# Kernel optimization log

Hardware: AMD Instinct MI355X
Metric: run time of the kernel (lower is better)

Reference implementation:

```python
import jax, jax.numpy as jnp
import numpy as np

EMBED_DIM = 1024
NUM_HEADS = 16
HEAD_DIM = EMBED_DIM // NUM_HEADS  # 64
SCALING = 0.125
T, B = 2048, 2


def setup_inputs() -> dict:
    key = jax.random.key(0)
    k_q, k_len, k_w1, k_b1, k_w2, k_b2 = jax.random.split(key, 6)
    query = jax.random.normal(k_q, (T, B, EMBED_DIM), dtype=jnp.float32)
    # realistic padding: each sequence has a valid length in [T//2, T)
    lengths = jax.random.randint(k_len, (B,), T // 2, T)
    key_padding_mask = jnp.arange(T)[None, :] >= lengths[:, None]  # [B, T] bool, True = pad
    s1 = 1.0 / np.sqrt(EMBED_DIM)
    W_in = jax.random.uniform(k_w1, (3 * EMBED_DIM, EMBED_DIM), jnp.float32, -s1, s1)
    b_in = jax.random.uniform(k_b1, (3 * EMBED_DIM,), jnp.float32, -s1, s1)
    W_out = jax.random.uniform(k_w2, (EMBED_DIM, EMBED_DIM), jnp.float32, -s1, s1)
    b_out = jax.random.uniform(k_b2, (EMBED_DIM,), jnp.float32, -s1, s1)
    return {"query": query, "key_padding_mask": key_padding_mask,
            "W_in": W_in, "b_in": b_in, "W_out": W_out, "b_out": b_out}


def reference(query, key_padding_mask, W_in, b_in, W_out, b_out):
    # query: [T, B, E]; key_padding_mask: [B, S] bool (True = padded key)
    t, b, e = query.shape
    h, hd = NUM_HEADS, HEAD_DIM
    proj = query @ W_in.T + b_in                      # [T, B, 3E]
    q, k, v = jnp.split(proj, 3, axis=-1)             # each [T, B, E]
    q = q * SCALING

    def to_bh(x):  # [T, B, E] -> [B*H, T, hd], matching torch view+transpose
        return x.reshape(t, b * h, hd).transpose(1, 0, 2)

    q, k, v = to_bh(q), to_bh(k), to_bh(v)
    attn_weights = jnp.einsum('bth,bsh->bts', q, k)   # [B*H, T, S]
    attn_weights = attn_weights.reshape(b, h, t, t)
    attn_weights = jnp.where(key_padding_mask[:, None, None, :], -jnp.inf, attn_weights)
    # softmax computed in float32 then cast back, as in the original
    attn_weights = jax.nn.softmax(attn_weights.astype(jnp.float32), axis=-1).astype(query.dtype)
    # dropout p=0 (eval/inference) -> identity
    attn = jnp.einsum('bhts,bhsd->bhtd', attn_weights, v.reshape(b, h, t, hd))  # [B,H,T,hd]
    attn = attn.reshape(b * h, t, hd).transpose(1, 0, 2).reshape(t, b, e)       # [T,B,E]
    return attn @ W_out.T + b_out
```

## Files before the change

### kernel.cpp

```cpp
#include <hip/hip_runtime.h>
#include <hip/hip_bf16.h>
#include <stdint.h>
#include <stddef.h>

typedef __hip_bfloat16 bf16;
typedef __attribute__((ext_vector_type(4))) float f32x4;
typedef __attribute__((ext_vector_type(8))) short s16x8;
typedef __attribute__((ext_vector_type(4))) short s16x4;

#define AS1 __attribute__((address_space(1)))
#define AS3 __attribute__((address_space(3)))

__device__ __forceinline__ void async_ld16(const void* g, void* l) {
  __builtin_amdgcn_global_load_lds((AS1 void*)g, (AS3 void*)l, 16, 0, 0);
}

#if __has_builtin(__builtin_amdgcn_exp2f)
#define EXP2F(x) __builtin_amdgcn_exp2f(x)
#else
#define EXP2F(x) exp2f(x)
#endif

__device__ __forceinline__ unsigned pk_bf16(float a, float b) {
  unsigned ua = __builtin_bit_cast(unsigned, a);
  unsigned ub = __builtin_bit_cast(unsigned, b);
  ua += 0x7FFFu + ((ua >> 16) & 1u);
  ub += 0x7FFFu + ((ub >> 16) & 1u);
  return (ua >> 16) | (ub & 0xFFFF0000u);
}

__device__ __forceinline__ unsigned pk_trunc(float a, float b) {
  return __builtin_amdgcn_perm(__builtin_bit_cast(unsigned, b),
                               __builtin_bit_cast(unsigned, a), 0x07060302u);
}

__global__ __launch_bounds__(256) void convert_all_kernel(const float* __restrict__ q_src,
                                                          const float* __restrict__ wi_src,
                                                          const float* __restrict__ wo_src,
                                                          bf16* __restrict__ q_dst,
                                                          bf16* __restrict__ wi_dst,
                                                          bf16* __restrict__ wo_dst,
                                                          const void* __restrict__ mask,
                                                          int* __restrict__ lengths) {
  int blk = blockIdx.x;
  if (blk >= 4096) {
    __shared__ int s_any;
    __shared__ int s_cnt[256];
    const int tid = threadIdx.x;
    const int b = blk - 4096;
    const unsigned char* m8 = (const unsigned char*)mask;
    if (tid == 0) s_any = 0;
    __syncthreads();
    int local = 0;
    for (int i = tid; i < 4096; i += 256) local |= m8[i];
    if (local) atomicOr(&s_any, 1);
    __syncthreads();
    int cnt = 0;
    if (s_any) {
      for (int t = tid; t < 2048; t += 256) cnt += (m8[b * 2048 + t] == 0) ? 1 : 0;
    } else {
      const int* m32 = (const int*)mask;
      for (int t = tid; t < 2048; t += 256) cnt += (m32[b * 2048 + t] == 0) ? 1 : 0;
    }
    s_cnt[tid] = cnt;
    __syncthreads();
    for (int s = 128; s > 0; s >>= 1) {
      if (tid < s) s_cnt[tid] += s_cnt[tid + s];
      __syncthreads();
    }
    if (tid == 0) lengths[b] = s_cnt[0];
    return;
  }
  const float* src;
  bf16* dst;
  int base;
  if (blk < 2048)      { src = q_src;  dst = q_dst;  base = blk * 2048; }
  else if (blk < 3584) { src = wi_src; dst = wi_dst; base = (blk - 2048) * 2048; }
  else                 { src = wo_src; dst = wo_dst; base = (blk - 3584) * 2048; }
  int i = base + threadIdx.x * 8;
  float4 a = *(const float4*)(src + i);
  float4 b = *(const float4*)(src + i + 4);
  unsigned u[4];
  u[0] = pk_bf16(a.x, a.y); u[1] = pk_bf16(a.z, a.w);
  u[2] = pk_bf16(b.x, b.y); u[3] = pk_bf16(b.z, b.w);
  *(uint4*)(dst + i) = *(const uint4*)u;
}

__global__ __launch_bounds__(256) void gemm_qkv(const bf16* __restrict__ X,
                                                const bf16* __restrict__ W,
                                                const float* __restrict__ bias,
                                                bf16* __restrict__ Qd,
                                                bf16* __restrict__ Kd,
                                                bf16* __restrict__ Vt) {
  __shared__ bf16 smem[128 * 64 * 2];
  bf16* As = smem;
  bf16* Bs = smem + 8192;
  const int K = 1024;
  const int id = blockIdx.x;
  const int xcd = id & 7;
  const int local = id >> 3;
  const int nloc = local % 3;
  const int by = local / 3;
  const int m0 = by * 128;
  const int n0 = (xcd * 3 + nloc) * 128;
  const int tid = threadIdx.x;
  const int wave = tid >> 6, lane = tid & 63;
  const int col = lane & 15, quad = lane >> 4;
  const int wm = wave & 1, wn = wave >> 1;

  f32x4 acc[4][4];
#pragma unroll
  for (int mi = 0; mi < 4; mi++)
#pragma unroll
    for (int ni = 0; ni < 4; ni++) acc[mi][ni] = (f32x4){0.f, 0.f, 0.f, 0.f};

  const bf16* gA[4];
  const bf16* gB[4];
  char* ldA[4];
  char* ldB[4];
#pragma unroll
  for (int i = 0; i < 4; i++) {
    const int c = tid + 256 * i;
    const int row = c >> 3;
    const int j = (c & 7) ^ (row & 7);
    gA[i] = X + (size_t)(m0 + row) * K + j * 8;
    gB[i] = W + (size_t)(n0 + row) * K + j * 8;
    ldA[i] = (char*)As + (size_t)(wave * 64 + 256 * i) * 16;
    ldB[i] = (char*)Bs + (size_t)(wave * 64 + 256 * i) * 16;
  }

  for (int k0 = 0; k0 < K; k0 += 64) {
#pragma unroll
    for (int i = 0; i < 4; i++) async_ld16(gA[i] + k0, ldA[i]);
#pragma unroll
    for (int i = 0; i < 4; i++) async_ld16(gB[i] + k0, ldB[i]);
    __syncthreads();
#pragma unroll
    for (int kh = 0; kh < 2; kh++) {
      s16x8 af[4], bfr[4];
#pragma unroll
      for (int mi = 0; mi < 4; mi++) {
        const int row = wm * 64 + mi * 16 + col;
        af[mi] = *(const s16x8*)((char*)As + row * 128 + (((kh << 2) | quad) ^ (row & 7)) * 16);
      }
#pragma unroll
      for (int ni = 0; ni < 4; ni++) {
        const int row = wn * 64 + ni * 16 + col;
        bfr[ni] = *(const s16x8*)((char*)Bs + row * 128 + (((kh << 2) | quad) ^ (row & 7)) * 16);
      }
#pragma unroll
      for (int mi = 0; mi < 4; mi++)
#pragma unroll
        for (int ni = 0; ni < 4; ni++)
          acc[mi][ni] = __builtin_amdgcn_mfma_f32_16x16x32_bf16(af[mi], bfr[ni], acc[mi][ni], 0, 0, 0);
    }
    __syncthreads();
  }

  const float QSCALE = 0.125f * 1.4426950408889634f;
  if (n0 < 2048) {
    bf16* dstb = (n0 < 1024) ? Qd : Kd;
    const float sc = (n0 < 1024) ? QSCALE : 1.0f;
#pragma unroll
    for (int mi = 0; mi < 4; mi++)
#pragma unroll
      for (int ni = 0; ni < 4; ni++)
#pragma unroll
        for (int r = 0; r < 4; r++) {
          int m = m0 + wm * 64 + mi * 16 + quad * 4 + r;
          int n = n0 + wn * 64 + ni * 16 + col;
          float v = (acc[mi][ni][r] + bias[n]) * sc;
          int e = n & 1023, hh = e >> 6, d = e & 63;
          int t = m >> 1, b = m & 1;
          int bh = b * 16 + hh;
          dstb[((size_t)bh * 2048 + t) * 64 + d] = __float2bfloat16(v);
        }
  } else {
    const int hh0 = (n0 - 2048) >> 6;
#pragma unroll
    for (int mi = 0; mi < 4; mi++) {
      const int s0i = wm * 32 + mi * 8 + quad * 2;
      const int perm0 = ((s0i >> 2) & 3) * 16 + (s0i >> 4) * 4 + (s0i & 3);
#pragma unroll
      for (int ni = 0; ni < 4; ni++) {
        const int n = n0 + wn * 64 + ni * 16 + col;
        const float bv = bias[n];
        const int d = ni * 16 + col;
#pragma unroll
        for (int b = 0; b < 2; b++) {
          float v0 = acc[mi][ni][b] + bv;
          float v1 = acc[mi][ni][b + 2] + bv;
          const int p = b * 2 + wn;
          *(unsigned*)((char*)smem + (p * 4096 + d * 64 + perm0) * 2) = pk_bf16(v0, v1);
        }
      }
    }
    __syncthreads();
    const int bh = (wave >> 1) * 16 + hh0 + (wave & 1);
    bf16* dstp = Vt + (size_t)bh * 131072 + (m0 >> 7) * 4096;
    const char* srcp = (const char*)smem + wave * 8192;
#pragma unroll
    for (int j = 0; j < 8; j++) {
      s16x8 v = *(const s16x8*)(srcp + j * 1024 + lane * 16);
      *(s16x8*)(dstp + j * 512 + lane * 8) = v;
    }
  }
}

__global__ __launch_bounds__(512, 4) void attn_kernel(const bf16* __restrict__ Qd,
                                                      const bf16* __restrict__ Kd,
                                                      const bf16* __restrict__ Vt,
                                                      const int* __restrict__ lengths,
                                                      bf16* __restrict__ attn_out) {
  __shared__ bf16 Ks[2][2][64 * 64];
  __shared__ bf16 Vs[2][2][64 * 64];

  const int id = blockIdx.x;
  const int slot = id >> 3;
  const int bh = (id & 7) * 4 + (slot & 3);
  const int qt0 = (slot >> 2) * 128;
  const int b = bh >> 4, h = bh & 15;

  const int tid = threadIdx.x;
  const int wave = tid >> 6, lane = tid & 63;
  const int half = wave >> 2, hw = wave & 3;
  const int col = lane & 15, quad = lane >> 4;
  const int len = lengths[b];
  const int nfull = len >> 6;
  const int rem = len & 63;
  const int nkt = nfull + (rem ? 1 : 0);
  const int nh0 = (nkt + 1) >> 1;
  const int first = half ? nh0 : 0;
  const int cnt = half ? (nkt - nh0) : nh0;

  s16x8 bq[2][2];
#pragma unroll
  for (int g = 0; g < 2; g++) {
    const bf16* qptr =
        Qd + ((size_t)bh * 2048 + qt0 + hw * 32 + g * 16 + col) * 64 + quad * 8;
    bq[g][0] = *(const s16x8*)(qptr);
    bq[g][1] = *(const s16x8*)(qptr + 32);
  }

  const int kbase0 = col * 128 + ((quad ^ (col & 7)) << 4);
  const int kbase1 = kbase0 ^ 64;
  const int vbase0 = col * 128 + (((quad << 1) ^ (col & 7)) << 4);
  const int vbase1 = vbase0 ^ 16;
  const int HBUF = half * 16384;

  const bf16* Kg = Kd + (size_t)bh * 2048 * 64;
  const bf16* Vg = Vt + (size_t)bh * 131072;
  const int c0 = hw * 128 + lane, c1 = c0 + 64;
  const int r0 = c0 >> 3, j0 = (c0 & 7) ^ (r0 & 7);
  const int r1 = c1 >> 3, j1 = (c1 & 7) ^ (r1 & 7);
  const bf16* gK0 = Kg + r0 * 64 + j0 * 8;
  const bf16* gK1 = Kg + r1 * 64 + j1 * 8;
  const bf16* gV0 = Vg + r0 * 64 + j0 * 8;
  const bf16* gV1 = Vg + r1 * 64 + j1 * 8;
  const int dst0 = (hw * 128) * 16, dst1 = (hw * 128 + 64) * 16;

  auto stage = [&](int kt, int BUF) {
    const int off = kt * 4096;
    async_ld16(gK0 + off, (char*)Ks + BUF + dst0);
    async_ld16(gK1 + off, (char*)Ks + BUF + dst1);
    async_ld16(gV0 + off, (char*)Vs + BUF + dst0);
    async_ld16(gV1 + off, (char*)Vs + BUF + dst1);
  };

  const s16x4 aOnes = {0x3F80, 0x3F80, 0x3F80, 0x3F80};
  const f32x4 Zf = (f32x4){0.f, 0.f, 0.f, 0.f};
  f32x4 lacc[2] = {Zf, Zf};
  f32x4 oaccT[2][4];
#pragma unroll
  for (int g = 0; g < 2; g++)
#pragma unroll
    for (int dt = 0; dt < 4; dt++) oaccT[g][dt] = Zf;

  auto score = [&](int BUF, f32x4 (&s0)[4], f32x4 (&s1)[4]) {
#pragma unroll
    for (int ti = 0; ti < 4; ti++) {
      const s16x8 ak0 = *(const s16x8*)((char*)Ks + BUF + ti * 2048 + kbase0);
      s0[ti] = __builtin_amdgcn_mfma_f32_16x16x32_bf16(ak0, bq[0][0], Zf, 0, 0, 0);
      s1[ti] = __builtin_amdgcn_mfma_f32_16x16x32_bf16(ak0, bq[1][0], Zf, 0, 0, 0);
      const s16x8 ak1 = *(const s16x8*)((char*)Ks + BUF + ti * 2048 + kbase1);
      s0[ti] = __builtin_amdgcn_mfma_f32_16x16x32_bf16(ak1, bq[0][1], s0[ti], 0, 0, 0);
      s1[ti] = __builtin_amdgcn_mfma_f32_16x16x32_bf16(ak1, bq[1][1], s1[ti], 0, 0, 0);
    }
  };
  auto accum = [&](int BUF, s16x4 (&bP0)[4], s16x4 (&bP1)[4]) {
#pragma unroll
    for (int ti = 0; ti < 4; ti++) {
      lacc[0] = __builtin_amdgcn_mfma_f32_16x16x16bf16_1k(aOnes, bP0[ti], lacc[0], 0, 0, 0);
      lacc[1] = __builtin_amdgcn_mfma_f32_16x16x16bf16_1k(aOnes, bP1[ti], lacc[1], 0, 0, 0);
    }
#pragma unroll
    for (int dt = 0; dt < 4; dt++) {
#pragma unroll
      for (int sh = 0; sh < 2; sh++) {
        const s16x8 av = *(const s16x8*)((char*)Vs + BUF + dt * 2048 + (sh ? vbase1 : vbase0));
        const s16x4 alo = __builtin_shufflevector(av, av, 0, 1, 2, 3);
        const s16x4 ahi = __builtin_shufflevector(av, av, 4, 5, 6, 7);
        oaccT[0][dt] = __builtin_amdgcn_mfma_f32_16x16x16bf16_1k(alo, bP0[sh * 2], oaccT[0][dt], 0, 0, 0);
        oaccT[0][dt] = __builtin_amdgcn_mfma_f32_16x16x16bf16_1k(ahi, bP0[sh * 2 + 1], oaccT[0][dt], 0, 0, 0);
        oaccT[1][dt] = __builtin_amdgcn_mfma_f32_16x16x16bf16_1k(alo, bP1[sh * 2], oaccT[1][dt], 0, 0, 0);
        oaccT[1][dt] = __builtin_amdgcn_mfma_f32_16x16x16bf16_1k(ahi, bP1[sh * 2 + 1], oaccT[1][dt], 0, 0, 0);
      }
    }
  };

  auto tile_full = [&](int BUF) {
    f32x4 s0[4], s1[4];
    score(BUF, s0, s1);
    s16x4 bP0[4], bP1[4];
#pragma unroll
    for (int ti = 0; ti < 4; ti++) {
      uint2 u0 = {pk_trunc(EXP2F(s0[ti][0]), EXP2F(s0[ti][1])),
                  pk_trunc(EXP2F(s0[ti][2]), EXP2F(s0[ti][3]))};
      bP0[ti] = __builtin_bit_cast(s16x4, u0);
      uint2 u1 = {pk_trunc(EXP2F(s1[ti][0]), EXP2F(s1[ti][1])),
                  pk_trunc(EXP2F(s1[ti][2]), EXP2F(s1[ti][3]))};
      bP1[ti] = __builtin_bit_cast(s16x4, u1);
    }
    accum(BUF, bP0, bP1);
  };

  auto tile_mask = [&](int BUF) {
    f32x4 s0[4], s1[4];
    score(BUF, s0, s1);
    s16x4 bP0[4], bP1[4];
#pragma unroll
    for (int ti = 0; ti < 4; ti++) {
      const int sb = ti * 16 + quad * 4;
      float a0 = (sb + 0 < rem) ? EXP2F(s0[ti][0]) : 0.f;
      float a1 = (sb + 1 < rem) ? EXP2F(s0[ti][1]) : 0.f;
      float a2 = (sb + 2 < rem) ? EXP2F(s0[ti][2]) : 0.f;
      float a3 = (sb + 3 < rem) ? EXP2F(s0[ti][3]) : 0.f;
      uint2 u0 = {pk_trunc(a0, a1), pk_trunc(a2, a3)};
      bP0[ti] = __builtin_bit_cast(s16x4, u0);
      float c0m = (sb + 0 < rem) ? EXP2F(s1[ti][0]) : 0.f;
      float c1m = (sb + 1 < rem) ? EXP2F(s1[ti][1]) : 0.f;
      float c2m = (sb + 2 < rem) ? EXP2F(s1[ti][2]) : 0.f;
      float c3m = (sb + 3 < rem) ? EXP2F(s1[ti][3]) : 0.f;
      uint2 u1 = {pk_trunc(c0m, c1m), pk_trunc(c2m, c3m)};
      bP1[ti] = __builtin_bit_cast(s16x4, u1);
    }
    accum(BUF, bP0, bP1);
  };

  stage(first, HBUF);
  __syncthreads();
  for (int i = 0; i < nh0; i++) {
    if (i + 1 < cnt) stage(first + i + 1, HBUF + ((i + 1) & 1) * 8192);
    if (i < cnt) {
      const int kt = first + i;
      const int BUF = HBUF + (i & 1) * 8192;
      if (kt < nfull) tile_full(BUF); else tile_mask(BUF);
    }
    __syncthreads();
  }

  float* OF = (float*)Ks;
  float* LF = (float*)Vs;
  const int me = hw * 64 + lane;
  if (half == 1) {
#pragma unroll
    for (int g = 0; g < 2; g++) {
      LF[g * 256 + me] = lacc[g][0];
#pragma unroll
      for (int dt = 0; dt < 4; dt++)
#pragma unroll
        for (int r = 0; r < 4; r++)
          OF[(g * 16 + dt * 4 + r) * 256 + me] = oaccT[g][dt][r];
    }
  }
  __syncthreads();
  if (half == 0) {
#pragma unroll
    for (int g = 0; g < 2; g++) {
      const float linv = 1.0f / (lacc[g][0] + LF[g * 256 + me]);
      const int t = qt0 + hw * 32 + g * 16 + col;
      bf16* outp = attn_out + ((size_t)t * 2 + b) * 1024 + h * 64 + quad * 4;
#pragma unroll
      for (int dt = 0; dt < 4; dt++) {
        float o0 = (oaccT[g][dt][0] + OF[(g * 16 + dt * 4 + 0) * 256 + me]) * linv;
        float o1 = (oaccT[g][dt][1] + OF[(g * 16 + dt * 4 + 1) * 256 + me]) * linv;
        float o2 = (oaccT[g][dt][2] + OF[(g * 16 + dt * 4 + 2) * 256 + me]) * linv;
        float o3 = (oaccT[g][dt][3] + OF[(g * 16 + dt * 4 + 3) * 256 + me]) * linv;
        uint2 u = {pk_bf16(o0, o1), pk_bf16(o2, o3)};
        *(uint2*)(outp + dt * 16) = u;
      }
    }
  }
}

__global__ __launch_bounds__(256) void gemm_out(const bf16* __restrict__ Aa,
                                                const bf16* __restrict__ W,
                                                const float* __restrict__ bias,
                                                float* __restrict__ out) {
  __shared__ bf16 Bs[128 * 64];
  __shared__ bf16 As[64 * 64];
  const int K = 1024;
  const int m0 = blockIdx.y * 64, n0 = blockIdx.x * 128;
  const int tid = threadIdx.x;
  const int wave = tid >> 6, lane = tid & 63;
  const int col = lane & 15, quad = lane >> 4;

  f32x4 acc[8];
#pragma unroll
  for (int ni = 0; ni < 8; ni++) acc[ni] = (f32x4){0.f, 0.f, 0.f, 0.f};

  const bf16* gB[4];
  char* ldsB[4];
#pragma unroll
  for (int i = 0; i < 4; i++) {
    const int c = tid + 256 * i;
    const int row = c >> 3;
    const int j = (c & 7) ^ (row & 7);
    gB[i] = W + (size_t)(n0 + row) * K + j * 8;
    ldsB[i] = (char*)Bs + (size_t)(wave * 64 + 256 * i) * 16;
  }
  const bf16* gA[2];
  char* ldsA[2];
#pragma unroll
  for (int i = 0; i < 2; i++) {
    const int c = tid + 256 * i;
    const int row = c >> 3;
    const int j = (c & 7) ^ (row & 7);
    gA[i] = Aa + (size_t)(m0 + row) * K + j * 8;
    ldsA[i] = (char*)As + (size_t)(wave * 64 + 256 * i) * 16;
  }

  for (int k0 = 0; k0 < K; k0 += 64) {
#pragma unroll
    for (int i = 0; i < 4; i++) async_ld16(gB[i] + k0, ldsB[i]);
#pragma unroll
    for (int i = 0; i < 2; i++) async_ld16(gA[i] + k0, ldsA[i]);
    __syncthreads();
    const int arow = wave * 16 + col;
    const int abase = arow * 128 + ((quad ^ (arow & 7)) << 4);
    const s16x8 af0 = *(const s16x8*)((char*)As + abase);
    const s16x8 af1 = *(const s16x8*)((char*)As + (abase ^ 64));
#pragma unroll
    for (int ni = 0; ni < 8; ni++) {
      const int brow = ni * 16 + col;
      const int bbase = brow * 128 + ((quad ^ (brow & 7)) << 4);
      const s16x8 b0 = *(const s16x8*)((char*)Bs + bbase);
      acc[ni] = __builtin_amdgcn_mfma_f32_16x16x32_bf16(af0, b0, acc[ni], 0, 0, 0);
      const s16x8 b1 = *(const s16x8*)((char*)Bs + (bbase ^ 64));
      acc[ni] = __builtin_amdgcn_mfma_f32_16x16x32_bf16(af1, b1, acc[ni], 0, 0, 0);
    }
    __syncthreads();
  }

#pragma unroll
  for (int ni = 0; ni < 8; ni++)
#pragma unroll
    for (int r = 0; r < 4; r++) {
      int m = m0 + wave * 16 + quad * 4 + r;
      int n = n0 + ni * 16 + col;
      out[(size_t)m * 1024 + n] = acc[ni][r] + bias[n];
    }
}

extern "C" void kernel_launch(void* const* d_in, const int* in_sizes, int n_in,
                              void* d_out, int out_size, void* d_ws, size_t ws_size,
                              hipStream_t stream) {
  (void)in_sizes; (void)n_in; (void)out_size; (void)ws_size;
  const float* query = (const float*)d_in[0];
  const void*  mask  = d_in[1];
  const float* W_in  = (const float*)d_in[2];
  const float* b_in  = (const float*)d_in[3];
  const float* W_out = (const float*)d_in[4];
  const float* b_out = (const float*)d_in[5];
  float* out = (float*)d_out;

  char* ws = (char*)d_ws;
  bf16* Xbf    = (bf16*)(ws);
  bf16* attnb  = (bf16*)(ws);
  bf16* Winbf  = (bf16*)(ws + 8388608);
  bf16* Woutbf = (bf16*)(ws + 8388608 + 6291456);
  bf16* Qd     = (bf16*)(ws + 16777216);
  bf16* Kd     = (bf16*)(ws + 25165824);
  bf16* Vt     = (bf16*)(ws + 33554432);
  int*  lens   = (int*)(ws + 41943040);

  convert_all_kernel<<<4098, 256, 0, stream>>>(query, W_in, W_out, Xbf, Winbf, Woutbf,
                                               mask, lens);
  gemm_qkv<<<768, 256, 0, stream>>>(Xbf, Winbf, b_in, Qd, Kd, Vt);
  attn_kernel<<<512, 512, 0, stream>>>(Qd, Kd, Vt, lens, attnb);
  gemm_out<<<dim3(8, 64), 256, 0, stream>>>(attnb, Woutbf, b_out, out);
}
```

Before: 189.3 us.

## Shrink QKV GEMM M-tile to 64 rows and re-layout V tiles for attention

```diff
diff --git a/kernel.cpp b/kernel.cpp
--- a/kernel.cpp
+++ b/kernel.cpp
@@ -86,70 +86,72 @@
   *(uint4*)(dst + i) = *(const uint4*)u;
 }
 
-__global__ __launch_bounds__(256) void gemm_qkv(const bf16* __restrict__ X,
-                                                const bf16* __restrict__ W,
-                                                const float* __restrict__ bias,
-                                                bf16* __restrict__ Qd,
-                                                bf16* __restrict__ Kd,
-                                                bf16* __restrict__ Vt) {
-  __shared__ bf16 smem[128 * 64 * 2];
+__global__ __launch_bounds__(256, 5) void gemm_qkv(const bf16* __restrict__ X,
+                                                   const bf16* __restrict__ W,
+                                                   const float* __restrict__ bias,
+                                                   bf16* __restrict__ Qd,
+                                                   bf16* __restrict__ Kd,
+                                                   bf16* __restrict__ Vt) {
+  __shared__ bf16 smem[(64 + 128) * 64];
   bf16* As = smem;
-  bf16* Bs = smem + 8192;
+  bf16* Bs = smem + 4096;
   const int K = 1024;
   const int id = blockIdx.x;
-  const int xcd = id & 7;
-  const int local = id >> 3;
-  const int nloc = local % 3;
-  const int by = local / 3;
-  const int m0 = by * 128;
-  const int n0 = (xcd * 3 + nloc) * 128;
+  const int mt = id & 63, nt = id >> 6;
+  const int m0 = mt * 64, n0 = nt * 128;
   const int tid = threadIdx.x;
   const int wave = tid >> 6, lane = tid & 63;
   const int col = lane & 15, quad = lane >> 4;
   const int wm = wave & 1, wn = wave >> 1;
 
-  f32x4 acc[4][4];
-#pragma unroll
-  for (int mi = 0; mi < 4; mi++)
+  f32x4 acc[2][4];
+#pragma unroll
+  for (int mi = 0; mi < 2; mi++)
 #pragma unroll
     for (int ni = 0; ni < 4; ni++) acc[mi][ni] = (f32x4){0.f, 0.f, 0.f, 0.f};
 
-  const bf16* gA[4];
+  const bf16* gA[2];
+  char* ldA[2];
+#pragma unroll
+  for (int i = 0; i < 2; i++) {
+    const int c = tid + 256 * i;
+    const int row = c >> 3;
+    const int j = (c & 7) ^ (row & 7);
+    gA[i] = X + (size_t)(m0 + row) * K + j * 8;
+    ldA[i] = (char*)As + (size_t)(wave * 64 + 256 * i) * 16;
+  }
   const bf16* gB[4];
-  char* ldA[4];
   char* ldB[4];
 #pragma unroll
   for (int i = 0; i < 4; i++) {
     const int c = tid + 256 * i;
     const int row = c >> 3;
     const int j = (c & 7) ^ (row & 7);
-    gA[i] = X + (size_t)(m0 + row) * K + j * 8;
     gB[i] = W + (size_t)(n0 + row) * K + j * 8;
-    ldA[i] = (char*)As + (size_t)(wave * 64 + 256 * i) * 16;
     ldB[i] = (char*)Bs + (size_t)(wave * 64 + 256 * i) * 16;
   }
 
   for (int k0 = 0; k0 < K; k0 += 64) {
 #pragma unroll
-    for (int i = 0; i < 4; i++) async_ld16(gA[i] + k0, ldA[i]);
+    for (int i = 0; i < 2; i++) async_ld16(gA[i] + k0, ldA[i]);
 #pragma unroll
     for (int i = 0; i < 4; i++) async_ld16(gB[i] + k0, ldB[i]);
     __syncthreads();
 #pragma unroll
     for (int kh = 0; kh < 2; kh++) {
-      s16x8 af[4], bfr[4];
-#pragma unroll
-      for (int mi = 0; mi < 4; mi++) {
-        const int row = wm * 64 + mi * 16 + col;
-        af[mi] = *(const s16x8*)((char*)As + row * 128 + (((kh << 2) | quad) ^ (row & 7)) * 16);
+      s16x8 af[2], bfr[4];
+#pragma unroll
+      for (int mi = 0; mi < 2; mi++) {
+        const int arow = wm * 32 + mi * 16 + col;
+        af[mi] = *(const s16x8*)((char*)As + arow * 128 + ((((kh << 2) | quad) ^ (arow & 7)) << 4));
       }
 #pragma unroll
       for (int ni = 0; ni < 4; ni++) {
-        const int row = wn * 64 + ni * 16 + col;
-        bfr[ni] = *(const s16x8*)((char*)Bs + row * 128 + (((kh << 2) | quad) ^ (row & 7)) * 16);
+        const int brow = wn * 64 + ni * 16 + col;
+        bfr[ni] = *(const s16x8*)((char*)Bs + brow * 128 + ((((kh << 2) | quad) ^ (brow & 7)) << 4));
       }
 #pragma unroll
-      for (int mi = 0; mi < 4; mi++)
+      for (int mi = 0; mi < 2; mi++)
 #pragma unroll
         for (int ni = 0; ni < 4; ni++)
           acc[mi][ni] = __builtin_amdgcn_mfma_f32_16x16x32_bf16(af[mi], bfr[ni], acc[mi][ni], 0, 0, 0);
@@ -158,16 +160,16 @@
   }
 
   const float QSCALE = 0.125f * 1.4426950408889634f;
-  if (n0 < 2048) {
-    bf16* dstb = (n0 < 1024) ? Qd : Kd;
-    const float sc = (n0 < 1024) ? QSCALE : 1.0f;
-#pragma unroll
-    for (int mi = 0; mi < 4; mi++)
+  if (nt < 16) {
+    bf16* dstb = (nt < 8) ? Qd : Kd;
+    const float sc = (nt < 8) ? QSCALE : 1.0f;
+#pragma unroll
+    for (int mi = 0; mi < 2; mi++)
 #pragma unroll
       for (int ni = 0; ni < 4; ni++)
 #pragma unroll
         for (int r = 0; r < 4; r++) {
-          int m = m0 + wm * 64 + mi * 16 + quad * 4 + r;
+          int m = m0 + wm * 32 + mi * 16 + quad * 4 + r;
           int n = n0 + wn * 64 + ni * 16 + col;
           float v = (acc[mi][ni][r] + bias[n]) * sc;
           int e = n & 1023, hh = e >> 6, d = e & 63;
@@ -176,33 +178,34 @@
           dstb[((size_t)bh * 2048 + t) * 64 + d] = __float2bfloat16(v);
         }
   } else {
-    const int hh0 = (n0 - 2048) >> 6;
-#pragma unroll
-    for (int mi = 0; mi < 4; mi++) {
-      const int s0i = wm * 32 + mi * 8 + quad * 2;
-      const int perm0 = ((s0i >> 2) & 3) * 16 + (s0i >> 4) * 4 + (s0i & 3);
+    const int hh0 = (nt - 16) * 2;
+#pragma unroll
+    for (int mi = 0; mi < 2; mi++) {
+      const int s0 = wm * 16 + mi * 8 + quad * 2;
+      const int off0 = ((s0 >> 2) & 3) * 8 + (s0 >> 4) * 4 + (s0 & 3);
 #pragma unroll
       for (int ni = 0; ni < 4; ni++) {
         const int n = n0 + wn * 64 + ni * 16 + col;
         const float bv = bias[n];
-        const int d = ni * 16 + col;
+        const int dfull = wn * 64 + ni * 16 + col;
+        const int hh_rel = dfull >> 6, dd = dfull & 63;
 #pragma unroll
         for (int b = 0; b < 2; b++) {
           float v0 = acc[mi][ni][b] + bv;
           float v1 = acc[mi][ni][b + 2] + bv;
-          const int p = b * 2 + wn;
-          *(unsigned*)((char*)smem + (p * 4096 + d * 64 + perm0) * 2) = pk_bf16(v0, v1);
+          const int p = b * 2 + hh_rel;
+          *(unsigned*)((char*)smem + ((p * 2048) + dd * 32 + off0) * 2) = pk_bf16(v0, v1);
         }
       }
     }
     __syncthreads();
     const int bh = (wave >> 1) * 16 + hh0 + (wave & 1);
-    bf16* dstp = Vt + (size_t)bh * 131072 + (m0 >> 7) * 4096;
-    const char* srcp = (const char*)smem + wave * 8192;
-#pragma unroll
-    for (int j = 0; j < 8; j++) {
-      s16x8 v = *(const s16x8*)(srcp + j * 1024 + lane * 16);
-      *(s16x8*)(dstp + j * 512 + lane * 8) = v;
+    bf16* dstp = Vt + (size_t)bh * 131072 + mt * 2048;
+    const char* srcp = (const char*)smem + wave * 4096;
+#pragma unroll
+    for (int jj = 0; jj < 4; jj++) {
+      s16x8 v = *(const s16x8*)(srcp + jj * 1024 + lane * 16);
+      *(s16x8*)(dstp + jj * 512 + lane * 8) = v;
     }
   }
 }
@@ -244,8 +247,6 @@
 
   const int kbase0 = col * 128 + ((quad ^ (col & 7)) << 4);
   const int kbase1 = kbase0 ^ 64;
-  const int vbase0 = col * 128 + (((quad << 1) ^ (col & 7)) << 4);
-  const int vbase1 = vbase0 ^ 16;
   const int HBUF = half * 16384;
 
   const bf16* Kg = Kd + (size_t)bh * 2048 * 64;
@@ -255,8 +256,8 @@
   const int r1 = c1 >> 3, j1 = (c1 & 7) ^ (r1 & 7);
   const bf16* gK0 = Kg + r0 * 64 + j0 * 8;
   const bf16* gK1 = Kg + r1 * 64 + j1 * 8;
-  const bf16* gV0 = Vg + r0 * 64 + j0 * 8;
-  const bf16* gV1 = Vg + r1 * 64 + j1 * 8;
+  const bf16* gV0 = Vg + (j0 >> 2) * 2048 + r0 * 32 + (j0 & 3) * 8;
+  const bf16* gV1 = Vg + (j1 >> 2) * 2048 + r1 * 32 + (j1 & 3) * 8;
   const int dst0 = (hw * 128) * 16, dst1 = (hw * 128 + 64) * 16;
 
   auto stage = [&](int kt, int BUF) {
@@ -297,7 +298,7 @@
     for (int dt = 0; dt < 4; dt++) {
 #pragma unroll
       for (int sh = 0; sh < 2; sh++) {
-        const s16x8 av = *(const s16x8*)((char*)Vs + BUF + dt * 2048 + (sh ? vbase1 : vbase0));
+        const s16x8 av = *(const s16x8*)((char*)Vs + BUF + dt * 2048 + (sh ? kbase1 : kbase0));
         const s16x4 alo = __builtin_shufflevector(av, av, 0, 1, 2, 3);
         const s16x4 ahi = __builtin_shufflevector(av, av, 4, 5, 6, 7);
         oaccT[0][dt] = __builtin_amdgcn_mfma_f32_16x16x16bf16_1k(alo, bP0[sh * 2], oaccT[0][dt], 0, 0, 0);
@@ -486,7 +487,7 @@
 
   convert_all_kernel<<<4098, 256, 0, stream>>>(query, W_in, W_out, Xbf, Winbf, Woutbf,
                                                mask, lens);
-  gemm_qkv<<<768, 256, 0, stream>>>(Xbf, Winbf, b_in, Qd, Kd, Vt);
+  gemm_qkv<<<1536, 256, 0, stream>>>(Xbf, Winbf, b_in, Qd, Kd, Vt);
   attn_kernel<<<512, 512, 0, stream>>>(Qd, Kd, Vt, lens, attnb);
   gemm_out<<<dim3(8, 64), 256, 0, stream>>>(attnb, Woutbf, b_out, out);
 }
```

After: 183.5 us, median of 2. 1.03x faster.
